# Optimization experiments

Measured on AMD Instinct MI355X. Metric: run time of the kernel, lower is better.

The kernel has to match this reference:

```python
import jax, jax.numpy as jnp
import numpy as np

S, B, H = 2048, 2, 2048
NH = 16
HD = H // NH
SCALE = HD ** -0.5


def setup_inputs() -> dict:
    key = jax.random.key(0)
    ks = jax.random.split(key, 5)
    sigma = 0.02
    return {
        "x": jax.random.normal(ks[0], (S, B, H), dtype=jnp.float32),
        "wq": jax.random.normal(ks[1], (H, H), dtype=jnp.float32) * sigma,
        "wk": jax.random.normal(ks[2], (H, H), dtype=jnp.float32) * sigma,
        "wv": jax.random.normal(ks[3], (H, H), dtype=jnp.float32) * sigma,
        "wo": jax.random.normal(ks[4], (H, H), dtype=jnp.float32) * sigma,
    }


def reference(x, wq, wk, wv, wo):
    # x: [s, b, h]; F.linear(x, W) == x @ W.T
    q = x @ wq.T
    k = x @ wk.T
    v = x @ wv.T
    s, b, _ = q.shape
    # [s, b, h] -> [b, nh, s, hd]
    def split_heads(t):
        return t.reshape(s, b, NH, HD).transpose(1, 2, 0, 3)
    q, k, v = split_heads(q), split_heads(k), split_heads(v)
    scores = jnp.einsum("bhqd,bhkd->bhqk", q, k) * SCALE
    attn = jax.nn.softmax(scores.astype(jnp.float32), axis=-1).astype(q.dtype)
    out = jnp.einsum("bhqk,bhkd->bhqd", attn, v)
    # [b, nh, s, hd] -> [s, b, h]
    out = out.transpose(2, 0, 1, 3).reshape(s, b, NH * HD)
    return out @ wo.T
```

## Files before the change

kernel.cpp:

```cpp
#include <hip/hip_runtime.h>

typedef __bf16 bf16;
typedef __bf16 bf16x8 __attribute__((ext_vector_type(8)));
typedef float f32x4 __attribute__((ext_vector_type(4)));
typedef float f32x16 __attribute__((ext_vector_type(16)));
typedef unsigned int uint;
typedef uint uint2v __attribute__((ext_vector_type(2)));

#define GLOAD16(g, l)                                                        \
  __builtin_amdgcn_global_load_lds(                                          \
      (const __attribute__((address_space(1))) void*)(g),                    \
      (__attribute__((address_space(3))) void*)(l), 16, 0, 0)

__device__ inline uint pack_bf16(float a, float b) {
  union { bf16 h[2]; uint u; } x;
  x.h[0] = (bf16)a; x.h[1] = (bf16)b;
  return x.u;
}

__global__ void cast_f32_to_bf16(const float* __restrict__ in,
                                 bf16* __restrict__ out, int n8, float scale) {
  int i = blockIdx.x * blockDim.x + threadIdx.x;
  if (i >= n8) return;
  const float4* p = reinterpret_cast<const float4*>(in) + (size_t)i * 2;
  float4 a = p[0], b = p[1];
  bf16x8 o;
  o[0] = (bf16)(a.x * scale); o[1] = (bf16)(a.y * scale);
  o[2] = (bf16)(a.z * scale); o[3] = (bf16)(a.w * scale);
  o[4] = (bf16)(b.x * scale); o[5] = (bf16)(b.y * scale);
  o[6] = (bf16)(b.z * scale); o[7] = (bf16)(b.w * scale);
  *reinterpret_cast<bf16x8*>(out + (size_t)i * 8) = o;
}

__global__ void cast4(const float* __restrict__ x, const float* __restrict__ wq,
                      const float* __restrict__ wk, const float* __restrict__ wv,
                      bf16* __restrict__ xb, bf16* __restrict__ wqk,
                      bf16* __restrict__ wvb, float qscale) {
  int i = blockIdx.x * blockDim.x + threadIdx.x;
  const float* src;
  bf16* dst;
  float s = 1.0f;
  int j;
  if (i < 1048576) {
    src = x; dst = xb; j = i;
  } else {
    int k = i - 1048576;
    int r = k >> 19;
    j = k & 524287;
    src = r == 0 ? wq : r == 1 ? wk : wv;
    dst = r == 0 ? wqk : r == 1 ? wqk + 4194304 : wvb;
    s = r == 0 ? qscale : 1.0f;
  }
  const float4* p = reinterpret_cast<const float4*>(src) + (size_t)j * 2;
  float4 a = p[0], b = p[1];
  bf16x8 o;
  o[0] = (bf16)(a.x * s); o[1] = (bf16)(a.y * s);
  o[2] = (bf16)(a.z * s); o[3] = (bf16)(a.w * s);
  o[4] = (bf16)(b.x * s); o[5] = (bf16)(b.y * s);
  o[6] = (bf16)(b.z * s); o[7] = (bf16)(b.w * s);
  *reinterpret_cast<bf16x8*>(dst + (size_t)j * 8) = o;
}

template <typename OT>
__global__ __launch_bounds__(512, 2) void gemm_nt_256(
    const bf16* __restrict__ A, const bf16* __restrict__ B, OT* __restrict__ C,
    int K, int lda, int ldb, int ldc, long bsB, long bsC, long cSplit) {
  extern __shared__ char sh[];
  const int t = threadIdx.x;
  const int w = t >> 6, lane = t & 63;
  const int l15 = lane & 15, l4 = lane >> 4;
  const int wr = w >> 1, wc = w & 1;
  const int gx = gridDim.x, gy = gridDim.y;
  const int nwg = gx * gy;
  const int bid = blockIdx.y * gx + blockIdx.x;
  const int fid = (bid & 7) * (nwg >> 3) + (bid >> 3);
  const int by = fid / gx, bx = fid - by * gx;
  const int m0 = by * 256;
  const int n0 = bx * 128;
  const bf16* Bg = B + (size_t)blockIdx.z * bsB;
  OT* Cg = C + (size_t)blockIdx.z * bsC + ((n0 & 2048) ? cSplit : 0);

  int sRow[4], sCol[4];
#pragma unroll
  for (int i = 0; i < 4; i++) {
    int sB_ = (i * 512 + t) * 16;
    int row = sB_ >> 7;
    int ge = (sB_ ^ ((row & 7) << 4)) >> 1;
    sRow[i] = ge >> 6;
    sCol[i] = ge & 63;
  }

  const int NT = K >> 6;
  f32x4 acc[4][4] = {};

  auto stage = [&](int tt) {
    char* dst = sh + (size_t)(tt % 3) * 49152;
    const int k0 = tt * 64;
#pragma unroll
    for (int i = 0; i < 4; i++)
      GLOAD16(A + (size_t)(m0 + sRow[i]) * lda + k0 + sCol[i],
              dst + (i * 512 + w * 64) * 16);
#pragma unroll
    for (int i = 0; i < 2; i++)
      GLOAD16(Bg + (size_t)(n0 + sRow[i]) * ldb + k0 + sCol[i],
              dst + 32768 + (i * 512 + w * 64) * 16);
  };

  stage(0);
  stage(1);
  for (int tt = 0; tt < NT; ++tt) {
    if (tt < NT - 1)
      asm volatile("s_waitcnt vmcnt(6)" ::: "memory");
    else
      asm volatile("s_waitcnt vmcnt(0)" ::: "memory");
    __builtin_amdgcn_s_barrier();

    const char* Ab = sh + (size_t)(tt % 3) * 49152;
    const char* Bb = Ab + 32768;
    bf16x8 bfr[4][2];
#pragma unroll
    for (int n = 0; n < 4; n++)
#pragma unroll
      for (int kk = 0; kk < 2; kk++) {
        int row = wc * 64 + n * 16 + l15;
        int off = (row * 128 + kk * 64 + l4 * 16) ^ ((row & 7) << 4);
        bfr[n][kk] = *reinterpret_cast<const bf16x8*>(Bb + off);
      }
    bf16x8 af0[2][2];
#pragma unroll
    for (int m = 0; m < 2; m++)
#pragma unroll
      for (int kk = 0; kk < 2; kk++) {
        int row = wr * 64 + m * 16 + l15;
        int off = (row * 128 + kk * 64 + l4 * 16) ^ ((row & 7) << 4);
        af0[m][kk] = *reinterpret_cast<const bf16x8*>(Ab + off);
      }
    __builtin_amdgcn_s_setprio(1);
#pragma unroll
    for (int m = 0; m < 2; m++)
#pragma unroll
      for (int n = 0; n < 4; n++)
#pragma unroll
        for (int kk = 0; kk < 2; kk++)
          acc[m][n] = __builtin_amdgcn_mfma_f32_16x16x32_bf16(
              af0[m][kk], bfr[n][kk], acc[m][n], 0, 0, 0);
    __builtin_amdgcn_s_setprio(0);

    if (tt + 2 < NT) stage(tt + 2);

    bf16x8 af1[2][2];
#pragma unroll
    for (int m = 0; m < 2; m++)
#pragma unroll
      for (int kk = 0; kk < 2; kk++) {
        int row = wr * 64 + (2 + m) * 16 + l15;
        int off = (row * 128 + kk * 64 + l4 * 16) ^ ((row & 7) << 4);
        af1[m][kk] = *reinterpret_cast<const bf16x8*>(Ab + off);
      }
    __builtin_amdgcn_s_setprio(1);
#pragma unroll
    for (int m = 0; m < 2; m++)
#pragma unroll
      for (int n = 0; n < 4; n++)
#pragma unroll
        for (int kk = 0; kk < 2; kk++)
          acc[2 + m][n] = __builtin_amdgcn_mfma_f32_16x16x32_bf16(
              af1[m][kk], bfr[n][kk], acc[2 + m][n], 0, 0, 0);
    __builtin_amdgcn_s_setprio(0);
  }

#pragma unroll
  for (int m = 0; m < 4; m++)
#pragma unroll
    for (int n = 0; n < 4; n++)
#pragma unroll
      for (int j = 0; j < 4; j++) {
        int row = m0 + wr * 64 + m * 16 + l4 * 4 + j;
        int col = n0 + wc * 64 + n * 16 + l15;
        Cg[(size_t)row * ldc + col] = (OT)acc[m][n][j];
      }
}

__global__ __launch_bounds__(512, 2) void attn_fwd(
    const bf16* __restrict__ Q, const bf16* __restrict__ Kb,
    const bf16* __restrict__ Vt, bf16* __restrict__ O) {
  extern __shared__ char ash[];
  const int t = threadIdx.x, w = t >> 6, lane = t & 63;
  const int l31 = lane & 31, half = lane >> 5;
  const int bh = blockIdx.x;
  const int b = bh >> 4, h = bh & 15;
  const int sq0 = blockIdx.y * 256 + w * 32;
  const size_t hoff = (size_t)h * 128;
  const size_t bO = (size_t)b * 2048 + hoff;

  bf16x8 qf[8];
  {
    const bf16* qp = Q + ((size_t)(sq0 + l31) * 2 + b) * 2048 + hoff + half * 8;
#pragma unroll
    for (int dc = 0; dc < 8; dc++)
      qf[dc] = *reinterpret_cast<const bf16x8*>(qp + dc * 16);
  }

  const bf16* kp[2];
  const bf16* vp[2];
#pragma unroll
  for (int i = 0; i < 2; i++) {
    int s = i * 512 + t;
    int row = s >> 4, g = s & 15;
    int lg = g ^ (row & 15);
    kp[i] = Kb + ((size_t)row * 2 + b) * 2048 + hoff + lg * 8;
    int d = row * 2 + (lg >> 3);
    vp[i] = Vt + (bO + d) * 2048 + (lg & 7) * 8;
  }

  auto stage = [&](int slot, int sk0) {
    char* Kd = ash + (size_t)slot * 32768;
    char* Vd = Kd + 16384;
#pragma unroll
    for (int i = 0; i < 2; i++)
      GLOAD16(kp[i] + (size_t)sk0 * 4096, Kd + (i * 512 + w * 64) * 16);
#pragma unroll
    for (int i = 0; i < 2; i++)
      GLOAD16(vp[i] + sk0, Vd + (i * 512 + w * 64) * 16);
  };

  f32x16 acc_o[4] = {};
  float m_run = -3e38f, l_run = 0.f;

  stage(0, 0);
  stage(1, 64);

  for (int it = 0; it < 32; ++it) {
    if (it < 31)
      asm volatile("s_waitcnt vmcnt(4)" ::: "memory");
    else
      asm volatile("s_waitcnt vmcnt(0)" ::: "memory");
    __builtin_amdgcn_s_barrier();

    const char* ksb = ash + (size_t)(it % 3) * 32768;
    const char* vsb = ksb + 16384;

    f32x16 sc[2] = {};
    bf16x8 ka[4], kb_[4], kc[4];
    auto loadK = [&](bf16x8 (&dst)[4], int g) {
#pragma unroll
      for (int j = 0; j < 2; j++) {
        int dc = g * 2 + j;
        int kx = ((dc * 2 + half) ^ (l31 & 15)) << 4;
        dst[j * 2 + 0] = *reinterpret_cast<const bf16x8*>(ksb + (l31 << 8) + kx);
        dst[j * 2 + 1] =
            *reinterpret_cast<const bf16x8*>(ksb + ((32 + l31) << 8) + kx);
      }
    };
    auto mfmaK = [&](bf16x8 (&kf)[4], int g) {
#pragma unroll
      for (int j = 0; j < 2; j++) {
        sc[0] = __builtin_amdgcn_mfma_f32_32x32x16_bf16(kf[j * 2 + 0],
                                                        qf[g * 2 + j], sc[0], 0, 0, 0);
        sc[1] = __builtin_amdgcn_mfma_f32_32x32x16_bf16(kf[j * 2 + 1],
                                                        qf[g * 2 + j], sc[1], 0, 0, 0);
      }
    };
    loadK(ka, 0);
    loadK(kb_, 1);
    loadK(kc, 2);
    __builtin_amdgcn_s_setprio(1);
    mfmaK(ka, 0);
    loadK(ka, 3);
    mfmaK(kb_, 1);
    mfmaK(kc, 2);
    mfmaK(ka, 3);
    __builtin_amdgcn_s_setprio(0);

    if (it + 2 < 32) stage((it + 2) % 3, (it + 2) * 64);

    float red[8];
#pragma unroll
    for (int r = 0; r < 8; r++)
      red[r] = fmaxf(fmaxf(sc[0][r], sc[0][r + 8]),
                     fmaxf(sc[1][r], sc[1][r + 8]));
#pragma unroll
    for (int s = 4; s >= 1; s >>= 1)
#pragma unroll
      for (int r = 0; r < s; r++) red[r] = fmaxf(red[r], red[r + s]);
    float pmax = fmaxf(red[0], __shfl_xor(red[0], 32));

    if (!__all(pmax - m_run <= 11.0f)) {
      float mn = fmaxf(m_run, pmax);
      float f = exp2f(m_run - mn);
      m_run = mn;
      l_run *= f;
#pragma unroll
      for (int idx = 0; idx < 16; idx++) {
        float fr = __shfl(f, (idx & 3) + 8 * (idx >> 2) + half * 4);
#pragma unroll
        for (int dcb = 0; dcb < 4; dcb++) acc_o[dcb][idx] *= fr;
      }
    }

#pragma unroll
    for (int kt = 0; kt < 2; kt++)
#pragma unroll
      for (int r = 0; r < 16; r++) sc[kt][r] = exp2f(sc[kt][r] - m_run);
#pragma unroll
    for (int r = 0; r < 8; r++)
      red[r] = (sc[0][r] + sc[0][r + 8]) + (sc[1][r] + sc[1][r + 8]);
#pragma unroll
    for (int s = 4; s >= 1; s >>= 1)
#pragma unroll
      for (int r = 0; r < s; r++) red[r] += red[r + s];
    l_run += red[0] + __shfl_xor(red[0], 32);

    bf16x8 va[4], vb[4], vc[4];
    auto loadV = [&](bf16x8 (&dst)[4], int dcb) {
      int rp = dcb * 16 + (l31 >> 1);
      int pbit = (l31 & 1) << 3;
#pragma unroll
      for (int skc = 0; skc < 4; skc++)
        dst[skc] = *reinterpret_cast<const bf16x8*>(
            vsb + (rp << 8) + (((pbit + skc * 2 + half) ^ (l31 >> 1)) << 4));
    };
    loadV(va, 0);
    loadV(vb, 1);
    loadV(vc, 2);

    uint pa[4][4];
#pragma unroll
    for (int skc = 0; skc < 4; skc++) {
      int kt = skc >> 1, s8 = (skc & 1) * 8;
      uint pk01 = pack_bf16(sc[kt][s8 + 0], sc[kt][s8 + 1]);
      uint pk23 = pack_bf16(sc[kt][s8 + 2], sc[kt][s8 + 3]);
      uint pk45 = pack_bf16(sc[kt][s8 + 4], sc[kt][s8 + 5]);
      uint pk67 = pack_bf16(sc[kt][s8 + 6], sc[kt][s8 + 7]);
      uint2v r02 = __builtin_amdgcn_permlane32_swap(pk01, pk45, false, false);
      uint2v r13 = __builtin_amdgcn_permlane32_swap(pk23, pk67, false, false);
      pa[skc][0] = r02[0];
      pa[skc][1] = r13[0];
      pa[skc][2] = r02[1];
      pa[skc][3] = r13[1];
    }

    auto mfmaV = [&](bf16x8 (&vf)[4], int dcb) {
#pragma unroll
      for (int skc = 0; skc < 4; skc++) {
        union { uint u[4]; bf16x8 v; } af;
        af.u[0] = pa[skc][0]; af.u[1] = pa[skc][1];
        af.u[2] = pa[skc][2]; af.u[3] = pa[skc][3];
        acc_o[dcb] = __builtin_amdgcn_mfma_f32_32x32x16_bf16(
            af.v, vf[skc], acc_o[dcb], 0, 0, 0);
      }
    };
    __builtin_amdgcn_s_setprio(1);
    mfmaV(va, 0);
    loadV(va, 3);
    mfmaV(vb, 1);
    mfmaV(vc, 2);
    mfmaV(va, 3);
    __builtin_amdgcn_s_setprio(0);
  }

  float inv = 1.0f / l_run;
#pragma unroll
  for (int idx = 0; idx < 16; idx++) {
    int sr = (idx & 3) + 8 * (idx >> 2) + half * 4;
    float invr = __shfl(inv, sr);
    bf16* op = O + ((size_t)(sq0 + sr) * 2 + b) * 2048 + hoff + l31;
#pragma unroll
    for (int dcb = 0; dcb < 4; dcb++)
      op[dcb * 32] = (bf16)(acc_o[dcb][idx] * invr);
  }
}

extern "C" void kernel_launch(void* const* d_in, const int* in_sizes, int n_in,
                              void* d_out, int out_size, void* d_ws,
                              size_t ws_size, hipStream_t stream) {
  (void)in_sizes; (void)n_in; (void)out_size; (void)ws_size;
  const float* x  = (const float*)d_in[0];
  const float* wq = (const float*)d_in[1];
  const float* wk = (const float*)d_in[2];
  const float* wv = (const float*)d_in[3];
  const float* wo = (const float*)d_in[4];
  float* out = (float*)d_out;
  char* ws = (char*)d_ws;
  bf16* xb   = (bf16*)(ws);
  bf16* qb   = (bf16*)(ws + (1u << 24));
  bf16* kb   = (bf16*)(ws + (2u << 24));
  bf16* vt   = (bf16*)(ws + (3u << 24));
  bf16* wb   = (bf16*)(ws + (4u << 24));
  bf16* wqk  = vt;
  bf16* attn = xb;
  const float SCALE = 0.08838834764831845f * 1.4426950408889634f;
  const int SMEM = 3 * 49152;
  const int SMEM_A = 3 * 32768;
  const long CSPLIT = (long)(kb - qb) - 2048;

  hipFuncSetAttribute((const void*)gemm_nt_256<bf16>,
                      hipFuncAttributeMaxDynamicSharedMemorySize, SMEM);
  hipFuncSetAttribute((const void*)gemm_nt_256<float>,
                      hipFuncAttributeMaxDynamicSharedMemorySize, SMEM);
  hipFuncSetAttribute((const void*)attn_fwd,
                      hipFuncAttributeMaxDynamicSharedMemorySize, SMEM_A);

  cast4<<<10240, 256, 0, stream>>>(x, wq, wk, wv, xb, wqk, wb, SCALE);

  dim3 gqk(32, 16, 1);
  gemm_nt_256<bf16><<<gqk, 512, SMEM, stream>>>(xb, wqk, qb, 2048, 2048, 2048,
                                                2048, 0, 0, CSPLIT);

  dim3 g2(16, 8, 2);
  gemm_nt_256<bf16><<<g2, 512, SMEM, stream>>>(wb, xb, vt, 2048, 2048, 4096, 2048,
                                               2048L, 4194304L, 0);

  dim3 ga(32, 8);
  attn_fwd<<<ga, 512, SMEM_A, stream>>>(qb, kb, vt, attn);

  cast_f32_to_bf16<<<2048, 256, 0, stream>>>(wo, wb, 4194304 / 8, 1.0f);
  dim3 g1(16, 16, 1);
  gemm_nt_256<float><<<g1, 512, SMEM, stream>>>(attn, wb, out, 2048, 2048, 2048,
                                                2048, 0, 0, 0);
}
```

Baseline: 264.4 us.

## Split attention KV range across two blocks and merge partial outputs

Splits the key/value sequence into two halves processed by separate blocks (grid z=2), each writing normalized partial outputs plus running max/sum, and adds a merge kernel that combines them with log-sum-exp weights. The LDS pipeline drops from triple to double buffering, with an extra barrier before restaging, and launch bounds request 4 blocks per CU. This is meant to raise block count and occupancy for the 256-block attention grid. In exchange it adds an extra kernel launch, extra global traffic for the partials, and a second bf16 rounding of the output.

```diff
diff --git a/kernel.cpp b/kernel.cpp
--- a/kernel.cpp
+++ b/kernel.cpp
@@ -181,13 +181,16 @@
       }
 }
 
-__global__ __launch_bounds__(512, 2) void attn_fwd(
+__global__ __launch_bounds__(512, 4) void attn_fwd(
     const bf16* __restrict__ Q, const bf16* __restrict__ Kb,
-    const bf16* __restrict__ Vt, bf16* __restrict__ O) {
+    const bf16* __restrict__ Vt, bf16* __restrict__ P0,
+    bf16* __restrict__ P1, float2* __restrict__ ml) {
   extern __shared__ char ash[];
   const int t = threadIdx.x, w = t >> 6, lane = t & 63;
   const int l31 = lane & 31, half = lane >> 5;
   const int bh = blockIdx.x;
+  const int half_id = blockIdx.z;
+  const int base = half_id * 16;
   const int b = bh >> 4, h = bh & 15;
   const int sq0 = blockIdx.y * 256 + w * 32;
   const size_t hoff = (size_t)h * 128;
@@ -213,9 +216,10 @@
     vp[i] = Vt + (bO + d) * 2048 + (lg & 7) * 8;
   }
 
-  auto stage = [&](int slot, int sk0) {
+  auto stage = [&](int slot, int tileIdx) {
     char* Kd = ash + (size_t)slot * 32768;
     char* Vd = Kd + 16384;
+    int sk0 = tileIdx * 64;
 #pragma unroll
     for (int i = 0; i < 2; i++)
       GLOAD16(kp[i] + (size_t)sk0 * 4096, Kd + (i * 512 + w * 64) * 16);
@@ -227,17 +231,17 @@
   f32x16 acc_o[4] = {};
   float m_run = -3e38f, l_run = 0.f;
 
-  stage(0, 0);
-  stage(1, 64);
-
-  for (int it = 0; it < 32; ++it) {
-    if (it < 31)
+  stage(0, base);
+  stage(1, base + 1);
+
+  for (int li = 0; li < 16; ++li) {
+    if (li < 15)
       asm volatile("s_waitcnt vmcnt(4)" ::: "memory");
     else
       asm volatile("s_waitcnt vmcnt(0)" ::: "memory");
     __builtin_amdgcn_s_barrier();
 
-    const char* ksb = ash + (size_t)(it % 3) * 32768;
+    const char* ksb = ash + (size_t)(li & 1) * 32768;
     const char* vsb = ksb + 16384;
 
     f32x16 sc[2] = {};
@@ -271,8 +275,6 @@
     mfmaK(kc, 2);
     mfmaK(ka, 3);
     __builtin_amdgcn_s_setprio(0);
-
-    if (it + 2 < 32) stage((it + 2) % 3, (it + 2) * 64);
 
     float red[8];
 #pragma unroll
@@ -357,18 +359,53 @@
     mfmaV(vc, 2);
     mfmaV(va, 3);
     __builtin_amdgcn_s_setprio(0);
-  }
-
+
+    __builtin_amdgcn_s_barrier();
+    if (li + 2 < 16) stage(li & 1, base + li + 2);
+  }
+
+  bf16* Pd = half_id ? P1 : P0;
   float inv = 1.0f / l_run;
 #pragma unroll
   for (int idx = 0; idx < 16; idx++) {
     int sr = (idx & 3) + 8 * (idx >> 2) + half * 4;
     float invr = __shfl(inv, sr);
-    bf16* op = O + ((size_t)(sq0 + sr) * 2 + b) * 2048 + hoff + l31;
+    bf16* op = Pd + ((size_t)(sq0 + sr) * 2 + b) * 2048 + hoff + l31;
 #pragma unroll
     for (int dcb = 0; dcb < 4; dcb++)
       op[dcb * 32] = (bf16)(acc_o[dcb][idx] * invr);
   }
+  if (lane < 32) {
+    float2 v;
+    v.x = m_run;
+    v.y = l_run;
+    ml[(size_t)half_id * 65536 + bh * 2048 + sq0 + l31] = v;
+  }
+}
+
+__global__ void merge_halves(const bf16* __restrict__ P1,
+                             const float2* __restrict__ ml,
+                             bf16* __restrict__ Out) {
+  int i = blockIdx.x * blockDim.x + threadIdx.x;
+  int mlIdx = i >> 4;
+  int d0 = (i & 15) * 8;
+  int bh = mlIdx >> 11, qrow = mlIdx & 2047;
+  int b = bh >> 4, h = bh & 15;
+  size_t off = ((size_t)qrow * 2 + b) * 2048 + h * 128 + d0;
+  float2 a = ml[mlIdx];
+  float2 c = ml[65536 + mlIdx];
+  float mM = fmaxf(a.x, c.x);
+  float e0 = exp2f(a.x - mM) * a.y;
+  float e1 = exp2f(c.x - mM) * c.y;
+  float w0 = e0 / (e0 + e1);
+  float w1 = 1.0f - w0;
+  bf16x8 p0 = *reinterpret_cast<const bf16x8*>(Out + off);
+  bf16x8 p1 = *reinterpret_cast<const bf16x8*>(P1 + off);
+  bf16x8 o;
+#pragma unroll
+  for (int j = 0; j < 8; j++)
+    o[j] = (bf16)(w0 * (float)p0[j] + w1 * (float)p1[j]);
+  *reinterpret_cast<bf16x8*>(Out + off) = o;
 }
 
 extern "C" void kernel_launch(void* const* d_in, const int* in_sizes, int n_in,
@@ -389,9 +426,11 @@
   bf16* wb   = (bf16*)(ws + (4u << 24));
   bf16* wqk  = vt;
   bf16* attn = xb;
+  bf16* P1   = (bf16*)d_out;
+  float2* ml = (float2*)wb;
   const float SCALE = 0.08838834764831845f * 1.4426950408889634f;
   const int SMEM = 3 * 49152;
-  const int SMEM_A = 3 * 32768;
+  const int SMEM_A = 2 * 32768;
   const long CSPLIT = (long)(kb - qb) - 2048;
 
   hipFuncSetAttribute((const void*)gemm_nt_256<bf16>,
@@ -411,8 +450,9 @@
   gemm_nt_256<bf16><<<g2, 512, SMEM, stream>>>(wb, xb, vt, 2048, 2048, 4096, 2048,
                                                2048L, 4194304L, 0);
 
-  dim3 ga(32, 8);
-  attn_fwd<<<ga, 512, SMEM_A, stream>>>(qb, kb, vt, attn);
+  dim3 ga(32, 8, 2);
+  attn_fwd<<<ga, 512, SMEM_A, stream>>>(qb, kb, vt, attn, P1, ml);
+  merge_halves<<<4096, 256, 0, stream>>>(P1, ml, attn);
 
   cast_f32_to_bf16<<<2048, 256, 0, stream>>>(wo, wb, 4194304 / 8, 1.0f);
   dim3 g1(16, 16, 1);
```

New measurement: 629.8 us. +138.2%, slower.

## Use 256x256 tile GEMM kernel for fused QK projection

Applied to the files above, without the earlier changes.

Adds a new GEMM kernel with a 256x256 output tile, a 2x4 wave layout and double-buffered 64-wide K stages, and uses it for the combined Q/K projection in place of the 256x128 kernel. The larger tile raises arithmetic intensity and reuses each staged A and B tile across more MFMAs, cutting global and LDS traffic per flop. In exchange, each block needs 128 KB of LDS with one block per CU and more accumulator registers, and the grid drops to 256 blocks with only two pipeline stages, so latency hiding may suffer.

```diff
diff --git a/kernel.cpp b/kernel.cpp
--- a/kernel.cpp
+++ b/kernel.cpp
@@ -59,6 +59,102 @@
   o[4] = (bf16)(b.x * s); o[5] = (bf16)(b.y * s);
   o[6] = (bf16)(b.z * s); o[7] = (bf16)(b.w * s);
   *reinterpret_cast<bf16x8*>(dst + (size_t)j * 8) = o;
+}
+
+template <typename OT>
+__global__ __launch_bounds__(512, 1) void gemm_nt_256sq(
+    const bf16* __restrict__ A, const bf16* __restrict__ B, OT* __restrict__ C,
+    int K, int lda, int ldb, int ldc, long cSplit) {
+  extern __shared__ char sh[];
+  const int t = threadIdx.x;
+  const int w = t >> 6, lane = t & 63;
+  const int l15 = lane & 15, l4 = lane >> 4;
+  const int wr = w >> 2, wc = w & 3;
+  const int gx = gridDim.x, gy = gridDim.y;
+  const int nwg = gx * gy;
+  const int bid = blockIdx.y * gx + blockIdx.x;
+  const int fid = (bid & 7) * (nwg >> 3) + (bid >> 3);
+  const int by = fid / gx, bx = fid - by * gx;
+  const int m0 = by * 256, n0 = bx * 256;
+  OT* Cg = C + ((n0 & 2048) ? cSplit : 0);
+
+  int sRow[4], sCol[4];
+#pragma unroll
+  for (int i = 0; i < 4; i++) {
+    int sB_ = (i * 512 + t) * 16;
+    int row = sB_ >> 7;
+    int ge = (sB_ ^ ((row & 7) << 4)) >> 1;
+    sRow[i] = ge >> 6;
+    sCol[i] = ge & 63;
+  }
+
+  const int NT = K >> 6;
+  f32x4 acc[8][4] = {};
+
+  auto stage = [&](int tt) {
+    char* dst = sh + (size_t)(tt & 1) * 65536;
+    const int k0 = tt * 64;
+#pragma unroll
+    for (int i = 0; i < 4; i++)
+      GLOAD16(A + (size_t)(m0 + sRow[i]) * lda + k0 + sCol[i],
+              dst + (i * 512 + w * 64) * 16);
+#pragma unroll
+    for (int i = 0; i < 4; i++)
+      GLOAD16(B + (size_t)(n0 + sRow[i]) * ldb + k0 + sCol[i],
+              dst + 32768 + (i * 512 + w * 64) * 16);
+  };
+
+  stage(0);
+  for (int tt = 0; tt < NT; ++tt) {
+    asm volatile("s_waitcnt vmcnt(0)" ::: "memory");
+    __builtin_amdgcn_s_barrier();
+
+    const char* Ab = sh + (size_t)(tt & 1) * 65536;
+    const char* Bb = Ab + 32768;
+    bf16x8 bfr[4][2];
+#pragma unroll
+    for (int n = 0; n < 4; n++)
+#pragma unroll
+      for (int kk = 0; kk < 2; kk++) {
+        int row = wc * 64 + n * 16 + l15;
+        int off = (row * 128 + kk * 64 + l4 * 16) ^ ((row & 7) << 4);
+        bfr[n][kk] = *reinterpret_cast<const bf16x8*>(Bb + off);
+      }
+#pragma unroll
+    for (int mp = 0; mp < 4; mp++) {
+      bf16x8 af[2][2];
+#pragma unroll
+      for (int m = 0; m < 2; m++)
+#pragma unroll
+        for (int kk = 0; kk < 2; kk++) {
+          int row = wr * 128 + (mp * 2 + m) * 16 + l15;
+          int off = (row * 128 + kk * 64 + l4 * 16) ^ ((row & 7) << 4);
+          af[m][kk] = *reinterpret_cast<const bf16x8*>(Ab + off);
+        }
+      __builtin_amdgcn_s_setprio(1);
+#pragma unroll
+      for (int m = 0; m < 2; m++)
+#pragma unroll
+        for (int n = 0; n < 4; n++)
+#pragma unroll
+          for (int kk = 0; kk < 2; kk++)
+            acc[mp * 2 + m][n] = __builtin_amdgcn_mfma_f32_16x16x32_bf16(
+                af[m][kk], bfr[n][kk], acc[mp * 2 + m][n], 0, 0, 0);
+      __builtin_amdgcn_s_setprio(0);
+      if (mp == 0 && tt + 1 < NT) stage(tt + 1);
+    }
+  }
+
+#pragma unroll
+  for (int m = 0; m < 8; m++)
+#pragma unroll
+    for (int n = 0; n < 4; n++)
+#pragma unroll
+      for (int j = 0; j < 4; j++) {
+        int row = m0 + wr * 128 + m * 16 + l4 * 4 + j;
+        int col = n0 + wc * 64 + n * 16 + l15;
+        Cg[(size_t)row * ldc + col] = (OT)acc[m][n][j];
+      }
 }
 
 template <typename OT>
@@ -391,9 +487,12 @@
   bf16* attn = xb;
   const float SCALE = 0.08838834764831845f * 1.4426950408889634f;
   const int SMEM = 3 * 49152;
+  const int SMEM_QK = 2 * 65536;
   const int SMEM_A = 3 * 32768;
   const long CSPLIT = (long)(kb - qb) - 2048;
 
+  hipFuncSetAttribute((const void*)gemm_nt_256sq<bf16>,
+                      hipFuncAttributeMaxDynamicSharedMemorySize, SMEM_QK);
   hipFuncSetAttribute((const void*)gemm_nt_256<bf16>,
                       hipFuncAttributeMaxDynamicSharedMemorySize, SMEM);
   hipFuncSetAttribute((const void*)gemm_nt_256<float>,
@@ -403,9 +502,9 @@
 
   cast4<<<10240, 256, 0, stream>>>(x, wq, wk, wv, xb, wqk, wb, SCALE);
 
-  dim3 gqk(32, 16, 1);
-  gemm_nt_256<bf16><<<gqk, 512, SMEM, stream>>>(xb, wqk, qb, 2048, 2048, 2048,
-                                                2048, 0, 0, CSPLIT);
+  dim3 gqk(16, 16, 1);
+  gemm_nt_256sq<bf16><<<gqk, 512, SMEM_QK, stream>>>(xb, wqk, qb, 2048, 2048,
+                                                     2048, 2048, CSPLIT);
 
   dim3 g2(16, 8, 2);
   gemm_nt_256<bf16><<<g2, 512, SMEM, stream>>>(wb, xb, vt, 2048, 2048, 4096, 2048,
```

Result: faster. 245.4 us (median of 2 runs) (-7.2%).
